# Kernel tuning notes

Measured on AMD Instinct MI355X. Metric: run time of the kernel, lower is better.

## Reference

```python
import jax, jax.numpy as jnp
import numpy as np


def setup_inputs() -> dict:
    key = jax.random.key(0)
    ks = jax.random.split(key, 12)
    N, D, E = 50000, 64, 320000
    H0, H1, H2, OUT = 4 * D, 128, 128, 1  # edgemlp_size=[256,128,128], out_features=1
    h1 = jax.random.normal(ks[0], (N, D), dtype=jnp.float32)
    h2 = jax.random.normal(ks[1], (N, D), dtype=jnp.float32)
    src = jax.random.randint(ks[2], (E,), 0, N, dtype=jnp.int64)
    dst = jax.random.randint(ks[3], (E,), 0, N, dtype=jnp.int64)
    def lin_init(kw, kb, fan_in, fan_out):
        bound = 1.0 / np.sqrt(fan_in)
        W = jax.random.uniform(kw, (fan_out, fan_in), minval=-bound, maxval=bound, dtype=jnp.float32)
        b = jax.random.uniform(kb, (fan_out,), minval=-bound, maxval=bound, dtype=jnp.float32)
        return W, b
    W1, b1 = lin_init(ks[4], ks[5], H0, H1)
    W2, b2 = lin_init(ks[6], ks[7], H1, H2)
    W3, b3 = lin_init(ks[8], ks[9], H2, OUT)
    return {"h1": h1, "h2": h2, "src": src, "dst": dst,
            "W1": W1, "b1": b1, "W2": W2, "b2": b2, "W3": W3, "b3": b3}


def reference(h1, h2, src, dst, W1, b1, W2, b2, W3, b3):
    # Gather per-edge node features. NOTE: original code uses edges.src['h2']
    # for BOTH h2_u and h2_v (faithful to source), so h2 is gathered by src twice.
    h1_u = h1[src]            # [E, D]
    h1_v = h1[dst]            # [E, D]
    h2_u = h2[src]            # [E, D]
    h2_v = h2[src]            # [E, D]  (src, per original)
    h = jnp.concatenate([h1_u, h1_v, h2_u, h2_v], axis=1)  # [E, 4D]
    h = jax.nn.sigmoid(h @ W1.T + b1)
    h = jax.nn.sigmoid(h @ W2.T + b2)
    score = h @ W3.T + b3     # [E, out_features]
    return score
```

## Files before the change

### kernel.cpp

```cpp
#include <hip/hip_runtime.h>
#include <hip/hip_bf16.h>
#include <cstdint>


typedef __attribute__((ext_vector_type(8))) short bf16x8;
typedef __attribute__((ext_vector_type(4))) float f32x4;

__device__ __forceinline__ float sigmoid_fast(float x) {
    float e = __expf(-x);
    return __builtin_amdgcn_rcpf(1.0f + e);
}
__device__ __forceinline__ ushort f2bf_rne(float f) {
    uint32_t u = __float_as_uint(f);
    return (ushort)((u + 0x7fffu + ((u >> 16) & 1u)) >> 16);
}
__device__ __forceinline__ float bf2f_lo(uint32_t d) { return __uint_as_float(d << 16); }
__device__ __forceinline__ float bf2f_hi(uint32_t d) { return __uint_as_float(d & 0xffff0000u); }
__device__ __forceinline__ uint32_t packbf_rhu(float x, float y) {
    return ((__float_as_uint(x) + 0x8000u) >> 16) |
           ((__float_as_uint(y) + 0x8000u) & 0xffff0000u);
}

__global__ void prep_kernel(const float* __restrict__ W1, const float* __restrict__ W2,
                            ushort* __restrict__ WCF, ushort* __restrict__ WBF,
                            ushort* __restrict__ W2F) {
    int i = blockIdx.x * blockDim.x + threadIdx.x;
    if (i >= 16384) return;
    int j = i & 7, lf = (i >> 3) & 63, nt = (i >> 9) & 7, kk = i >> 12;
    int n = nt * 16 + (lf & 15);
    int kpos = kk * 32 + ((lf >> 4) << 3) + j;
    int ktrue = (kpos & ~31) | ((kpos >> 1) & 15) | ((kpos & 1) << 4);
    W2F[i] = f2bf_rne(W2[n * 128 + ktrue]);
    float v = (kpos < 64) ? W1[n * 256 + kpos]
                          : W1[n * 256 + 128 + (kpos - 64)] + W1[n * 256 + 192 + (kpos - 64)];
    WCF[i] = f2bf_rne(v);
    if (kk < 2) WBF[i] = f2bf_rne(W1[n * 256 + 64 + kpos]);
}

__global__ __launch_bounds__(256, 4) void node_kernel(
    const float* __restrict__ h1, const float* __restrict__ h2,
    const ushort* __restrict__ WCF, const ushort* __restrict__ WBF,
    const float* __restrict__ b1,
    uint32_t* __restrict__ Aout, uint32_t* __restrict__ Bout, int N)
{
    __shared__ __align__(16) ushort xt[64 * 136];
    const int tid = threadIdx.x, g = tid >> 6, ln = tid & 63;
    const int nl = ln & 15, q = ln >> 4;
    const int n0 = blockIdx.x * 64;
    const bool full = (n0 + 64 <= N);

    bf16x8 fa[4][2], fb[2][2];
    #pragma unroll
    for (int kk = 0; kk < 4; ++kk)
        #pragma unroll
        for (int nt = 0; nt < 2; ++nt)
            fa[kk][nt] = *(const bf16x8*)(WCF + (((kk * 8 + g * 2 + nt) * 64 + ln) << 3));
    #pragma unroll
    for (int kk = 0; kk < 2; ++kk)
        #pragma unroll
        for (int nt = 0; nt < 2; ++nt)
            fb[kk][nt] = *(const bf16x8*)(WBF + (((kk * 8 + g * 2 + nt) * 64 + ln) << 3));
    const float b1c0 = b1[g * 32 + nl], b1c1 = b1[g * 32 + 16 + nl];

    #pragma unroll
    for (int i = 0; i < 8; ++i) {
        int local = i * 256 + tid;
        int node = local >> 5;
        int kq = (local & 31) * 4;
        float4 x = make_float4(0.f, 0.f, 0.f, 0.f);
        if (full || n0 + node < N)
            x = (kq < 64) ? *(const float4*)(h1 + (size_t)(n0 + node) * 64 + kq)
                          : *(const float4*)(h2 + (size_t)(n0 + node) * 64 + (kq - 64));
        uint32_t d0 = packbf_rhu(x.x, x.y), d1 = packbf_rhu(x.z, x.w);
        *(uint2*)&xt[node * 136 + kq] = make_uint2(d0, d1);
    }
    __syncthreads();

    #pragma unroll
    for (int m = 0; m < 4; ++m) {
        f32x4 accA[2], accB[2];
        #pragma unroll
        for (int r = 0; r < 4; ++r) { accA[0][r] = accA[1][r] = accB[0][r] = accB[1][r] = 0.f; }
        const ushort* arow = &xt[(m * 16 + nl) * 136 + (q << 3)];
        #pragma unroll
        for (int kk = 0; kk < 4; ++kk) {
            bf16x8 a = *(const bf16x8*)(arow + kk * 32);
            accA[0] = __builtin_amdgcn_mfma_f32_16x16x32_bf16(a, fa[kk][0], accA[0], 0, 0, 0);
            accA[1] = __builtin_amdgcn_mfma_f32_16x16x32_bf16(a, fa[kk][1], accA[1], 0, 0, 0);
            if (kk < 2) {
                accB[0] = __builtin_amdgcn_mfma_f32_16x16x32_bf16(a, fb[kk][0], accB[0], 0, 0, 0);
                accB[1] = __builtin_amdgcn_mfma_f32_16x16x32_bf16(a, fb[kk][1], accB[1], 0, 0, 0);
            }
        }
        #pragma unroll
        for (int r = 0; r < 4; ++r) {
            int node = n0 + m * 16 + q * 4 + r;
            if (full || node < N) {
                Aout[(size_t)node * 64 + g * 16 + nl] = packbf_rhu(accA[0][r] + b1c0, accA[1][r] + b1c1);
                Bout[(size_t)node * 64 + g * 16 + nl] = packbf_rhu(accB[0][r], accB[1][r]);
            }
        }
    }
}

__global__ __launch_bounds__(256, 4) void edge_kernel(
    const uint32_t* __restrict__ Am, const uint32_t* __restrict__ Bm,
    const int* __restrict__ src, const int* __restrict__ dst,
    const ushort* __restrict__ W2F, const float* __restrict__ b2,
    const float* __restrict__ W3, const float* __restrict__ b3,
    float* __restrict__ out, int E, int ntiles)
{
    __shared__ __align__(16) ushort hlds[64 * 136];
    __shared__ float part[2][256];
    const int tid = threadIdx.x, g = tid >> 6, ln = tid & 63;
    const int nl = ln & 15, q = ln >> 4;
    const int el = g * 16 + (ln >> 2);
    const int p  = ln & 3;
    const int G  = gridDim.x;

    bf16x8 bfrag[8];
    #pragma unroll
    for (int kk = 0; kk < 4; ++kk)
        #pragma unroll
        for (int nt = 0; nt < 2; ++nt)
            bfrag[kk * 2 + nt] =
                *(const bf16x8*)(W2F + (((kk * 8 + g * 2 + nt) * 64 + ln) << 3));
    float b2c[2], w3c[2];
    #pragma unroll
    for (int nt = 0; nt < 2; ++nt) {
        int n = g * 32 + nt * 16 + nl;
        b2c[nt] = b2[n]; w3c[nt] = W3[n];
    }
    const float b3c = b3[0];

    uint4 ga[4], gb[4];
    int uB = 0, vB = 0;
    int t = blockIdx.x;
    if (t < ntiles) {
        int e0 = t * 64 + el;
        int u0 = 0, v0 = 0;
        if (e0 < E) { u0 = src[e0]; v0 = dst[e0]; }
        const uint32_t* ap = Am + (size_t)u0 * 64 + p * 4;
        const uint32_t* bp = Bm + (size_t)v0 * 64 + p * 4;
        #pragma unroll
        for (int r = 0; r < 4; ++r) {
            ga[r] = *(const uint4*)(ap + r * 16);
            gb[r] = *(const uint4*)(bp + r * 16);
        }
        int t1 = t + G;
        if (t1 < ntiles) {
            int e1 = t1 * 64 + el;
            if (e1 < E) { uB = src[e1]; vB = dst[e1]; }
        }
    }
    int buf = 0, prev = -1;
    for (; t < ntiles; t += G) {
        #pragma unroll
        for (int r = 0; r < 4; ++r) {
            uint32_t sa[4] = {ga[r].x, ga[r].y, ga[r].z, ga[r].w};
            uint32_t sb[4] = {gb[r].x, gb[r].y, gb[r].z, gb[r].w};
            uint32_t da[4];
            #pragma unroll
            for (int d = 0; d < 4; ++d) {
                float zl = bf2f_lo(sa[d]) + bf2f_lo(sb[d]);
                float zh = bf2f_hi(sa[d]) + bf2f_hi(sb[d]);
                da[d] = packbf_rhu(sigmoid_fast(zl), sigmoid_fast(zh));
            }
            *(uint4*)&hlds[el * 136 + r * 32 + p * 8] =
                make_uint4(da[0], da[1], da[2], da[3]);
        }
        int uC = 0, vC = 0;
        int t2 = t + 2 * G;
        if (t2 < ntiles) {
            int e2 = t2 * 64 + el;
            if (e2 < E) { uC = src[e2]; vC = dst[e2]; }
        }
        if (t + G < ntiles) {
            const uint32_t* ap = Am + (size_t)uB * 64 + p * 4;
            const uint32_t* bp = Bm + (size_t)vB * 64 + p * 4;
            #pragma unroll
            for (int r = 0; r < 4; ++r) {
                ga[r] = *(const uint4*)(ap + r * 16);
                gb[r] = *(const uint4*)(bp + r * 16);
            }
        }
        __syncthreads();

        if (prev >= 0 && tid < 64) {
            int e = prev * 64 + tid;
            if (e < E)
                out[e] = (part[buf ^ 1][tid] + part[buf ^ 1][64 + tid])
                       + (part[buf ^ 1][128 + tid] + part[buf ^ 1][192 + tid]) + b3c;
        }

        #pragma unroll
        for (int m = 0; m < 4; ++m) {
            f32x4 acc[2];
            #pragma unroll
            for (int r = 0; r < 4; ++r) { acc[0][r] = 0.f; acc[1][r] = 0.f; }
            const ushort* arow = &hlds[(m * 16 + nl) * 136 + (q << 3)];
            #pragma unroll
            for (int kk = 0; kk < 4; ++kk) {
                bf16x8 a = *(const bf16x8*)(arow + kk * 32);
                acc[0] = __builtin_amdgcn_mfma_f32_16x16x32_bf16(a, bfrag[kk * 2],     acc[0], 0, 0, 0);
                acc[1] = __builtin_amdgcn_mfma_f32_16x16x32_bf16(a, bfrag[kk * 2 + 1], acc[1], 0, 0, 0);
            }
            float pr[4] = {0.f, 0.f, 0.f, 0.f};
            #pragma unroll
            for (int nt = 0; nt < 2; ++nt)
                #pragma unroll
                for (int r = 0; r < 4; ++r)
                    pr[r] = fmaf(w3c[nt], sigmoid_fast(acc[nt][r] + b2c[nt]), pr[r]);
            #pragma unroll
            for (int r = 0; r < 4; ++r) {
                pr[r] += __shfl_xor(pr[r], 1, 16);
                pr[r] += __shfl_xor(pr[r], 2, 16);
                pr[r] += __shfl_xor(pr[r], 4, 16);
                pr[r] += __shfl_xor(pr[r], 8, 16);
            }
            if (nl == 0) {
                #pragma unroll
                for (int r = 0; r < 4; ++r)
                    part[buf][g * 64 + m * 16 + q * 4 + r] = pr[r];
            }
        }
        __syncthreads();
        uB = uC; vB = vC;
        prev = t; buf ^= 1;
    }
    if (prev >= 0 && tid < 64) {
        int e = prev * 64 + tid;
        if (e < E)
            out[e] = (part[buf ^ 1][tid] + part[buf ^ 1][64 + tid])
                   + (part[buf ^ 1][128 + tid] + part[buf ^ 1][192 + tid]) + b3c;
    }
}

__global__ void naive_kernel(
    const float* __restrict__ h1, const float* __restrict__ h2,
    const int* __restrict__ src, const int* __restrict__ dst,
    const float* __restrict__ W1, const float* __restrict__ b1,
    const float* __restrict__ W2, const float* __restrict__ b2,
    const float* __restrict__ W3, const float* __restrict__ b3,
    float* __restrict__ out, int E, int N)
{
    int e = blockIdx.x * blockDim.x + threadIdx.x;
    if (e >= E) return;
    int u = src[e], v = dst[e];
    float h[128];
    for (int j = 0; j < 128; ++j) {
        float z = b1[j];
        const float* wj = W1 + j * 256;
        for (int k = 0; k < 64; ++k) {
            z += wj[k] * h1[(size_t)u * 64 + k]
               + wj[64 + k] * h1[(size_t)v * 64 + k]
               + (wj[128 + k] + wj[192 + k]) * h2[(size_t)u * 64 + k];
        }
        h[j] = 1.0f / (1.0f + __expf(-z));
    }
    float gg[128];
    for (int j = 0; j < 128; ++j) {
        float z = b2[j];
        for (int k = 0; k < 128; ++k) z = fmaf(W2[j * 128 + k], h[k], z);
        gg[j] = 1.0f / (1.0f + __expf(-z));
    }
    float s = b3[0];
    for (int j = 0; j < 128; ++j) s = fmaf(W3[j], gg[j], s);
    out[e] = s;
}

extern "C" void kernel_launch(void* const* d_in, const int* in_sizes, int n_in,
                              void* d_out, int out_size, void* d_ws, size_t ws_size,
                              hipStream_t stream) {
    const float* h1 = (const float*)d_in[0];
    const float* h2 = (const float*)d_in[1];
    const int*  src = (const int*)d_in[2];
    const int*  dst = (const int*)d_in[3];
    const float* W1 = (const float*)d_in[4];
    const float* b1 = (const float*)d_in[5];
    const float* W2 = (const float*)d_in[6];
    const float* b2 = (const float*)d_in[7];
    const float* W3 = (const float*)d_in[8];
    const float* b3 = (const float*)d_in[9];
    float* out = (float*)d_out;

    const int N = in_sizes[0] / 64;
    const int E = in_sizes[2];

    size_t offA   = 0;
    size_t offB   = offA + (size_t)N * 64;
    size_t offWCF = offB + (size_t)N * 64;
    size_t offWBF = offWCF + 8192;
    size_t offW2F = offWBF + 4096;
    size_t totalF = offW2F + 8192;

    if (ws_size < totalF * sizeof(float)) {
        naive_kernel<<<(E + 255) / 256, 256, 0, stream>>>(
            h1, h2, src, dst, W1, b1, W2, b2, W3, b3, out, E, N);
        return;
    }

    float* ws = (float*)d_ws;
    ushort* WCF = (ushort*)(ws + offWCF);
    ushort* WBF = (ushort*)(ws + offWBF);
    ushort* W2F = (ushort*)(ws + offW2F);

    prep_kernel<<<64, 256, 0, stream>>>(W1, W2, WCF, WBF, W2F);
    node_kernel<<<(N + 63) / 64, 256, 0, stream>>>(
        h1, h2, WCF, WBF, b1, (uint32_t*)(ws + offA), (uint32_t*)(ws + offB), N);
    const int ntiles = (E + 63) / 64;
    const int nblk = ntiles < 2048 ? ntiles : 2048;
    edge_kernel<<<nblk, 256, 0, stream>>>(
        (const uint32_t*)(ws + offA), (const uint32_t*)(ws + offB), src, dst,
        W2F, b2, W3, b3, out, E, ntiles);
}
```

Measured before the change: 134.7 us.

## Make edge MLP wave-local via ds_bpermute, dropping LDS staging and block barriers

Each wavefront now owns 16 edges end to end. It builds its layer-2 A fragments through ds_bpermute register shuffles instead of writing to shared memory, and computes all 128 hidden columns itself with the full W2 held in registers. This removes the LDS tile, both __syncthreads per tile, and the cross-wave partial-sum buffer, and outputs are written directly as float4. In exchange, register pressure rises (32 B fragments per lane), occupancy is lowered to 2 blocks per CU, and the grid shrinks from 2048 to 512 blocks.

After: 130.6 us. 1.03x faster.

```diff
diff --git a/kernel.cpp b/kernel.cpp
--- a/kernel.cpp
+++ b/kernel.cpp
@@ -5,6 +5,7 @@
 
 typedef __attribute__((ext_vector_type(8))) short bf16x8;
 typedef __attribute__((ext_vector_type(4))) float f32x4;
+typedef __attribute__((ext_vector_type(4))) int   i32x4;
 
 __device__ __forceinline__ float sigmoid_fast(float x) {
     float e = __expf(-x);
@@ -103,32 +104,30 @@
     }
 }
 
-__global__ __launch_bounds__(256, 4) void edge_kernel(
+__global__ __launch_bounds__(256, 2) void edge_kernel(
     const uint32_t* __restrict__ Am, const uint32_t* __restrict__ Bm,
     const int* __restrict__ src, const int* __restrict__ dst,
     const ushort* __restrict__ W2F, const float* __restrict__ b2,
     const float* __restrict__ W3, const float* __restrict__ b3,
     float* __restrict__ out, int E, int ntiles)
 {
-    __shared__ __align__(16) ushort hlds[64 * 136];
-    __shared__ float part[2][256];
     const int tid = threadIdx.x, g = tid >> 6, ln = tid & 63;
     const int nl = ln & 15, q = ln >> 4;
-    const int el = g * 16 + (ln >> 2);
+    const int el = ln >> 2;
     const int p  = ln & 3;
     const int G  = gridDim.x;
-
-    bf16x8 bfrag[8];
+    const int sl = ((nl << 2) | q) << 2;
+
+    bf16x8 bfrag[4][8];
     #pragma unroll
     for (int kk = 0; kk < 4; ++kk)
         #pragma unroll
-        for (int nt = 0; nt < 2; ++nt)
-            bfrag[kk * 2 + nt] =
-                *(const bf16x8*)(W2F + (((kk * 8 + g * 2 + nt) * 64 + ln) << 3));
-    float b2c[2], w3c[2];
-    #pragma unroll
-    for (int nt = 0; nt < 2; ++nt) {
-        int n = g * 32 + nt * 16 + nl;
+        for (int nt = 0; nt < 8; ++nt)
+            bfrag[kk][nt] = *(const bf16x8*)(W2F + (((kk * 8 + nt) * 64 + ln) << 3));
+    float b2c[8], w3c[8];
+    #pragma unroll
+    for (int nt = 0; nt < 8; ++nt) {
+        int n = nt * 16 + nl;
         b2c[nt] = b2[n]; w3c[nt] = W3[n];
     }
     const float b3c = b3[0];
@@ -137,7 +136,7 @@
     int uB = 0, vB = 0;
     int t = blockIdx.x;
     if (t < ntiles) {
-        int e0 = t * 64 + el;
+        int e0 = t * 64 + g * 16 + el;
         int u0 = 0, v0 = 0;
         if (e0 < E) { u0 = src[e0]; v0 = dst[e0]; }
         const uint32_t* ap = Am + (size_t)u0 * 64 + p * 4;
@@ -149,30 +148,27 @@
         }
         int t1 = t + G;
         if (t1 < ntiles) {
-            int e1 = t1 * 64 + el;
+            int e1 = t1 * 64 + g * 16 + el;
             if (e1 < E) { uB = src[e1]; vB = dst[e1]; }
         }
     }
-    int buf = 0, prev = -1;
     for (; t < ntiles; t += G) {
+        i32x4 da[4];
         #pragma unroll
         for (int r = 0; r < 4; ++r) {
             uint32_t sa[4] = {ga[r].x, ga[r].y, ga[r].z, ga[r].w};
             uint32_t sb[4] = {gb[r].x, gb[r].y, gb[r].z, gb[r].w};
-            uint32_t da[4];
             #pragma unroll
             for (int d = 0; d < 4; ++d) {
                 float zl = bf2f_lo(sa[d]) + bf2f_lo(sb[d]);
                 float zh = bf2f_hi(sa[d]) + bf2f_hi(sb[d]);
-                da[d] = packbf_rhu(sigmoid_fast(zl), sigmoid_fast(zh));
-            }
-            *(uint4*)&hlds[el * 136 + r * 32 + p * 8] =
-                make_uint4(da[0], da[1], da[2], da[3]);
+                da[r][d] = (int)packbf_rhu(sigmoid_fast(zl), sigmoid_fast(zh));
+            }
         }
         int uC = 0, vC = 0;
         int t2 = t + 2 * G;
         if (t2 < ntiles) {
-            int e2 = t2 * 64 + el;
+            int e2 = t2 * 64 + g * 16 + el;
             if (e2 < E) { uC = src[e2]; vC = dst[e2]; }
         }
         if (t + G < ntiles) {
@@ -184,55 +180,44 @@
                 gb[r] = *(const uint4*)(bp + r * 16);
             }
         }
-        __syncthreads();
-
-        if (prev >= 0 && tid < 64) {
-            int e = prev * 64 + tid;
-            if (e < E)
-                out[e] = (part[buf ^ 1][tid] + part[buf ^ 1][64 + tid])
-                       + (part[buf ^ 1][128 + tid] + part[buf ^ 1][192 + tid]) + b3c;
-        }
-
-        #pragma unroll
-        for (int m = 0; m < 4; ++m) {
-            f32x4 acc[2];
-            #pragma unroll
-            for (int r = 0; r < 4; ++r) { acc[0][r] = 0.f; acc[1][r] = 0.f; }
-            const ushort* arow = &hlds[(m * 16 + nl) * 136 + (q << 3)];
-            #pragma unroll
-            for (int kk = 0; kk < 4; ++kk) {
-                bf16x8 a = *(const bf16x8*)(arow + kk * 32);
-                acc[0] = __builtin_amdgcn_mfma_f32_16x16x32_bf16(a, bfrag[kk * 2],     acc[0], 0, 0, 0);
-                acc[1] = __builtin_amdgcn_mfma_f32_16x16x32_bf16(a, bfrag[kk * 2 + 1], acc[1], 0, 0, 0);
-            }
-            float pr[4] = {0.f, 0.f, 0.f, 0.f};
-            #pragma unroll
-            for (int nt = 0; nt < 2; ++nt)
+        i32x4 pa[4];
+        #pragma unroll
+        for (int kk = 0; kk < 4; ++kk)
+            #pragma unroll
+            for (int j = 0; j < 4; ++j)
+                pa[kk][j] = __builtin_amdgcn_ds_bpermute(sl, da[kk][j]);
+
+        float pr[4] = {0.f, 0.f, 0.f, 0.f};
+        #pragma unroll
+        for (int nt = 0; nt < 8; ++nt) {
+            f32x4 acc = {0.f, 0.f, 0.f, 0.f};
+            #pragma unroll
+            for (int kk = 0; kk < 4; ++kk)
+                acc = __builtin_amdgcn_mfma_f32_16x16x32_bf16(
+                    __builtin_bit_cast(bf16x8, pa[kk]), bfrag[kk][nt], acc, 0, 0, 0);
+            #pragma unroll
+            for (int r = 0; r < 4; ++r)
+                pr[r] = fmaf(w3c[nt], sigmoid_fast(acc[r] + b2c[nt]), pr[r]);
+        }
+        #pragma unroll
+        for (int r = 0; r < 4; ++r) {
+            pr[r] += __shfl_xor(pr[r], 1, 16);
+            pr[r] += __shfl_xor(pr[r], 2, 16);
+            pr[r] += __shfl_xor(pr[r], 4, 16);
+            pr[r] += __shfl_xor(pr[r], 8, 16);
+        }
+        if (nl == 0) {
+            int e0 = t * 64 + g * 16 + q * 4;
+            if (e0 + 4 <= E) {
+                f32x4 v = {pr[0] + b3c, pr[1] + b3c, pr[2] + b3c, pr[3] + b3c};
+                *(f32x4*)(out + e0) = v;
+            } else {
                 #pragma unroll
                 for (int r = 0; r < 4; ++r)
-                    pr[r] = fmaf(w3c[nt], sigmoid_fast(acc[nt][r] + b2c[nt]), pr[r]);
-            #pragma unroll
-            for (int r = 0; r < 4; ++r) {
-                pr[r] += __shfl_xor(pr[r], 1, 16);
-                pr[r] += __shfl_xor(pr[r], 2, 16);
-                pr[r] += __shfl_xor(pr[r], 4, 16);
-                pr[r] += __shfl_xor(pr[r], 8, 16);
-            }
-            if (nl == 0) {
-                #pragma unroll
-                for (int r = 0; r < 4; ++r)
-                    part[buf][g * 64 + m * 16 + q * 4 + r] = pr[r];
-            }
-        }
-        __syncthreads();
+                    if (e0 + r < E) out[e0 + r] = pr[r] + b3c;
+            }
+        }
         uB = uC; vB = vC;
-        prev = t; buf ^= 1;
-    }
-    if (prev >= 0 && tid < 64) {
-        int e = prev * 64 + tid;
-        if (e < E)
-            out[e] = (part[buf ^ 1][tid] + part[buf ^ 1][64 + tid])
-                   + (part[buf ^ 1][128 + tid] + part[buf ^ 1][192 + tid]) + b3c;
     }
 }
 
@@ -309,7 +294,7 @@
     node_kernel<<<(N + 63) / 64, 256, 0, stream>>>(
         h1, h2, WCF, WBF, b1, (uint32_t*)(ws + offA), (uint32_t*)(ws + offB), N);
     const int ntiles = (E + 63) / 64;
-    const int nblk = ntiles < 2048 ? ntiles : 2048;
+    const int nblk = ntiles < 512 ? ntiles : 512;
     edge_kernel<<<nblk, 256, 0, stream>>>(
         (const uint32_t*)(ws + offA), (const uint32_t*)(ws + offB), src, dst,
         W2F, b2, W3, b3, out, E, ntiles);
```
